# Optimization experiments

Measured on AMD Instinct MI355X. Metric: run time of the kernel, lower is better.

The kernel has to match this reference:

```python
import jax, jax.numpy as jnp
import numpy as np

B, L, H = 2, 4096, 1024
ED, N, R, K = 2048, 16, 64, 4


def setup_inputs() -> dict:
    key = jax.random.key(0)
    ks = jax.random.split(key, 8)
    w = lambda i, shape, s=0.02: jax.random.normal(ks[i], shape, jnp.float32) * s
    # dt bias initialized like Mamba: inv-softplus of dt ~ logU(1e-3, 1e-1)
    dt = jnp.exp(jax.random.uniform(ks[7], (ED,)) * (np.log(0.1) - np.log(0.001)) + np.log(0.001))
    dt = jnp.clip(dt, 1e-4)
    inv_dt = dt + jnp.log(-jnp.expm1(-dt))
    A = jnp.broadcast_to(jnp.arange(1, N + 1, dtype=jnp.float32), (ED, N))
    return dict(
        x=jax.random.normal(ks[0], (B, L, H), jnp.float32),
        in_proj_w=w(1, (2 * ED, H)),
        conv_w=w(2, (ED, K), 0.2),
        conv_b=jnp.zeros((ED,), jnp.float32),
        x_proj_w=w(3, (R + 2 * N, ED)),
        dt_w=w(4, (ED, R), 64 ** -0.5),
        dt_b=inv_dt,
        A_log=jnp.log(A),
        D=jnp.ones((ED,), jnp.float32),
        out_proj_w=w(5, (H, ED)),
    )


def reference(x, in_proj_w, conv_w, conv_b, x_proj_w, dt_w, dt_b, A_log, D, out_proj_w):
    Bq, Lq, Hq = x.shape
    EDq, Kq = conv_w.shape
    Rq = dt_w.shape[1]
    Nq = A_log.shape[1]

    # in_proj -> [B, L, 2*ED]; chunk into hidden_states and gate
    xz = jnp.einsum('blh,eh->ble', x, in_proj_w)
    hs, gate = jnp.split(xz, 2, axis=-1)

    # causal depthwise conv1d along L (padding K-1 on the left), then SiLU
    hs_pad = jnp.pad(hs, ((0, 0), (Kq - 1, 0), (0, 0)))  # [B, L+K-1, ED]
    conv = conv_b
    for k in range(Kq):  # K=4, fixed small loop
        conv = conv + hs_pad[:, k:k + Lq, :] * conv_w[:, k]
    hs = jax.nn.silu(conv)  # [B, L, ED]

    # x_proj -> split into dt (rank R), B (N), C (N)
    ssm = jnp.einsum('ble,pe->blp', hs, x_proj_w)
    dtr, Bm, Cm = jnp.split(ssm, [Rq, Rq + Nq], axis=-1)

    # dt_proj + softplus (delta_softplus=True with delta_bias)
    delta = jax.nn.softplus(jnp.einsum('blr,er->ble', dtr, dt_w) + dt_b)  # [B,L,ED]

    A = -jnp.exp(A_log)  # [ED, N]

    # selective scan: h_t = exp(delta_t*A)*h_{t-1} + delta_t*B_t*u_t ; y_t = <h_t, C_t>
    def step(h, inp):
        d_t, B_t, C_t, u_t = inp  # [B,ED], [B,N], [B,N], [B,ED]
        dA = jnp.exp(d_t[..., None] * A)                      # [B,ED,N]
        h = dA * h + (d_t * u_t)[..., None] * B_t[:, None, :]  # [B,ED,N]
        y = jnp.einsum('ben,bn->be', h, C_t)                   # [B,ED]
        return h, y

    h0 = jnp.zeros((Bq, EDq, Nq), x.dtype)
    xs = (jnp.moveaxis(delta, 1, 0), jnp.moveaxis(Bm, 1, 0),
          jnp.moveaxis(Cm, 1, 0), jnp.moveaxis(hs, 1, 0))
    _, ys = jax.lax.scan(step, h0, xs)  # ys: [L, B, ED]

    y = jnp.moveaxis(ys, 0, 1) + hs * D      # skip term D*u
    y = y * jax.nn.silu(gate)                # gated output
    return jnp.einsum('ble,he->blh', y, out_proj_w)
```

## Files before the change

### kernel.cpp

```cpp
#include <hip/hip_runtime.h>


typedef float f32x4 __attribute__((ext_vector_type(4)));
typedef short short8 __attribute__((ext_vector_type(8)));
typedef unsigned short u16;

#define DEV __device__ __forceinline__

DEV float bf2f(u16 u) {
  union { unsigned int i; float f; } v; v.i = ((unsigned int)u) << 16; return v.f;
}
DEV u16 f2bf(float f) {
  union { float f; unsigned int i; } v; v.f = f;
  return (u16)((v.i + 0x7fffu + ((v.i >> 16) & 1u)) >> 16);
}

DEV void gload_lds16(const void* g, void* l) {
  __builtin_amdgcn_global_load_lds(
      (const __attribute__((address_space(1))) unsigned int*)g,
      (__attribute__((address_space(3))) unsigned int*)l, 16, 0, 0);
}

DEV void mfma_bf16(f32x4& d, short8 a, short8 b) {
  asm("v_mfma_f32_16x16x32_bf16 %0, %1, %2, %0" : "+v"(d) : "v"(a), "v"(b));
}

template <int BM, int BN, int WM, int WN, int BK, int EPI>
__global__ __launch_bounds__(256) void gemm_bt_kernel(
    const u16* __restrict__ A, const u16* __restrict__ Bw,
    int M, int N, int Kd,
    float* __restrict__ o_f32, u16* __restrict__ o_b16a,
    u16* __restrict__ o_b16b, const float* __restrict__ bias,
    float* __restrict__ oB, float* __restrict__ oC)
{
  constexpr int KSN = BK / 32;
  constexpr int CPR = BK / 8;
  constexpr int CPL = (CPR == 8) ? 3 : 2;
  constexpr int MFR = BM / WM / 16;
  constexpr int NFR = BN / WN / 16;
  constexpr int TA = BM * CPR;
  constexpr int TB = BN * CPR;
  __shared__ u16 lds[(BM + BN) * BK];

  const int tid  = threadIdx.x;
  const int wave = tid >> 6;
  const int lane = tid & 63;
  const int row  = lane & 15;
  const int g    = lane >> 4;
  const int key  = (CPR == 8) ? (row & 7) : ((row >> 1) & 3);
  const int rowBase = blockIdx.y * BM;
  const int colBase = blockIdx.x * BN;
  const int WROW = (wave / WN) * (BM / WM);
  const int WCOL = (wave % WN) * (BN / WN);

  f32x4 acc[MFR][NFR];
#pragma unroll
  for (int i = 0; i < MFR; ++i)
#pragma unroll
    for (int j = 0; j < NFR; ++j) acc[i][j] = (f32x4){0.f, 0.f, 0.f, 0.f};

  for (int kk = 0; kk < Kd; kk += BK) {
#pragma unroll
    for (int c0 = 0; c0 < TA; c0 += 256) {
      int ch = c0 + tid;
      if (ch < TA) {
        int r = ch >> CPL;
        int rk = (CPR == 8) ? (r & 7) : ((r >> 1) & 3);
        int gs = (ch & (CPR - 1)) ^ rk;
        gload_lds16(A + (size_t)(rowBase + r) * Kd + kk + gs * 8,
                    (void*)(lds + (c0 + wave * 64) * 8));
      }
    }
#pragma unroll
    for (int c0 = 0; c0 < TB; c0 += 256) {
      int ch = c0 + tid;
      if (ch < TB) {
        int r = ch >> CPL;
        int rk = (CPR == 8) ? (r & 7) : ((r >> 1) & 3);
        int gs = (ch & (CPR - 1)) ^ rk;
        gload_lds16(Bw + (size_t)(colBase + r) * Kd + kk + gs * 8,
                    (void*)(lds + BM * BK + (c0 + wave * 64) * 8));
      }
    }
    __syncthreads();
    short8 af[MFR][KSN], bfr[NFR][KSN];
#pragma unroll
    for (int mi = 0; mi < MFR; ++mi)
#pragma unroll
      for (int ks = 0; ks < KSN; ++ks)
        af[mi][ks] = *(const short8*)(lds + (WROW + mi * 16 + row) * BK +
                                      (((ks * 4 + g) ^ key) * 8));
#pragma unroll
    for (int ni = 0; ni < NFR; ++ni)
#pragma unroll
      for (int ks = 0; ks < KSN; ++ks)
        bfr[ni][ks] = *(const short8*)(lds + BM * BK + (WCOL + ni * 16 + row) * BK +
                                       (((ks * 4 + g) ^ key) * 8));
#pragma unroll
    for (int ks = 0; ks < KSN; ++ks)
#pragma unroll
      for (int mi = 0; mi < MFR; ++mi)
#pragma unroll
        for (int ni = 0; ni < NFR; ++ni)
          mfma_bf16(acc[mi][ni], af[mi][ks], bfr[ni][ks]);
    __syncthreads();
  }

#pragma unroll
  for (int mi = 0; mi < MFR; ++mi) {
#pragma unroll
    for (int ni = 0; ni < NFR; ++ni) {
      const int gcol = colBase + WCOL + ni * 16 + row;
#pragma unroll
      for (int r = 0; r < 4; ++r) {
        const int grow = rowBase + WROW + mi * 16 + g * 4 + r;
        float v = acc[mi][ni][r];
        if constexpr (EPI == 0) {
          o_f32[(size_t)grow * N + gcol] = v;
        } else if constexpr (EPI == 1) {
          if (gcol < 2048) o_b16a[(size_t)grow * 2048 + gcol] = f2bf(v);
          else             o_b16b[(size_t)grow * 2048 + (gcol - 2048)] = f2bf(v);
        } else if constexpr (EPI == 2) {
          if (gcol < 64)      o_b16a[(size_t)grow * 64 + gcol] = f2bf(v);
          else if (gcol < 80) oB[(size_t)grow * 16 + (gcol - 64)] = v;
          else                oC[(size_t)grow * 16 + (gcol - 80)] = v;
        } else {
          float x = v + bias[gcol];
          float sp = (x > 20.f) ? x : __logf(1.f + __expf(x));
          o_b16a[(size_t)grow * N + gcol] = f2bf(sp);
        }
      }
    }
  }
}

DEV void cvt8(const float* in, u16* out, int j) {
  const float4* p = (const float4*)(in + (size_t)j * 8);
  float4 a = p[0], b = p[1];
  float v[8] = {a.x, a.y, a.z, a.w, b.x, b.y, b.z, b.w};
  unsigned o[4];
#pragma unroll
  for (int q = 0; q < 4; ++q)
    o[q] = (unsigned)f2bf(v[2 * q]) | ((unsigned)f2bf(v[2 * q + 1]) << 16);
  *(uint4*)(out + (size_t)j * 8) = make_uint4(o[0], o[1], o[2], o[3]);
}

__global__ __launch_bounds__(256) void cvt_bf16_kernel(
    const float* __restrict__ in, u16* __restrict__ out, int n8)
{
  int i = blockIdx.x * 256 + threadIdx.x;
  if (i >= n8) return;
  cvt8(in, out, i);
}

__global__ __launch_bounds__(256) void cvt4_kernel(
    const float* __restrict__ a0, u16* __restrict__ o0, int n0,
    const float* __restrict__ a1, u16* __restrict__ o1, int n1,
    const float* __restrict__ a2, u16* __restrict__ o2, int n2,
    const float* __restrict__ a3, u16* __restrict__ o3, int n3)
{
  int i = blockIdx.x * 256 + threadIdx.x;
  if (i < n0)                { cvt8(a0, o0, i); return; }
  i -= n0;
  if (i < n1)                { cvt8(a1, o1, i); return; }
  i -= n1;
  if (i < n2)                { cvt8(a2, o2, i); return; }
  i -= n2;
  if (i < n3)                { cvt8(a3, o3, i); }
}

__global__ __launch_bounds__(256) void conv_silu_kernel(
    const u16* __restrict__ hsraw, const float* __restrict__ cw,
    const float* __restrict__ cb, u16* __restrict__ hsb)
{
  int idx = blockIdx.x * 256 + threadIdx.x;
  int e0 = (idx & 255) * 8;
  int t  = (idx >> 8) & 4095;
  int b  = idx >> 20;
  float acc[8];
  float wv[4][8];
#pragma unroll
  for (int j = 0; j < 8; ++j) acc[j] = cb[e0 + j];
#pragma unroll
  for (int k = 0; k < 4; ++k)
#pragma unroll
    for (int j = 0; j < 8; ++j) wv[k][j] = cw[(e0 + j) * 4 + k];
#pragma unroll
  for (int k = 0; k < 4; ++k) {
    int tt = t - 3 + k;
    if (tt < 0) continue;
    uint4 v4 = *(const uint4*)(hsraw + ((size_t)(b * 4096 + tt)) * 2048 + e0);
    unsigned arr[4] = {v4.x, v4.y, v4.z, v4.w};
#pragma unroll
    for (int q = 0; q < 4; ++q) {
      acc[2 * q]     += wv[k][2 * q]     * bf2f((u16)(arr[q] & 0xffffu));
      acc[2 * q + 1] += wv[k][2 * q + 1] * bf2f((u16)(arr[q] >> 16));
    }
  }
  unsigned o[4];
#pragma unroll
  for (int q = 0; q < 4; ++q) {
    float a0 = acc[2 * q], a1 = acc[2 * q + 1];
    a0 = a0 / (1.f + __expf(-a0));
    a1 = a1 / (1.f + __expf(-a1));
    o[q] = (unsigned)f2bf(a0) | ((unsigned)f2bf(a1) << 16);
  }
  *(uint4*)(hsb + ((size_t)(b * 4096 + t)) * 2048 + e0) = make_uint4(o[0], o[1], o[2], o[3]);
}

__global__ __launch_bounds__(256) void scan_phase1(
    const u16* __restrict__ deltab, const u16* __restrict__ hsb,
    const float* __restrict__ Bb, const float* __restrict__ alog,
    float* __restrict__ h_end, float* __restrict__ Ssum)
{
  __shared__ __align__(16) float Bs[64 * 16];
  const int tid = threadIdx.x;
  const int e = blockIdx.x * 256 + tid;
  const int c = blockIdx.y;
  const int b = blockIdx.z;
  const int t0 = c * 64;
  {
    const float* src = Bb + ((size_t)(b * 4096 + t0)) * 16;
#pragma unroll
    for (int k = 0; k < 4; ++k) Bs[tid + k * 256] = src[tid + k * 256];
  }
  float An[16];
  {
    const float4* ap = (const float4*)(alog + e * 16);
#pragma unroll
    for (int q = 0; q < 4; ++q) {
      float4 v = ap[q];
      An[4*q+0] = -__expf(v.x); An[4*q+1] = -__expf(v.y);
      An[4*q+2] = -__expf(v.z); An[4*q+3] = -__expf(v.w);
    }
  }
  __syncthreads();
  float h[16];
#pragma unroll
  for (int n = 0; n < 16; ++n) h[n] = 0.f;
  float sumd = 0.f;
  size_t base = ((size_t)(b * 4096 + t0)) * 2048 + e;
  float dd = bf2f(deltab[base]);
  float uu = bf2f(hsb[base]);
  for (int j = 0; j < 64; ++j) {
    int jn = (j < 63) ? j + 1 : 63;
    float d_nxt = bf2f(deltab[base + (size_t)jn * 2048]);
    float u_nxt = bf2f(hsb[base + (size_t)jn * 2048]);
    const float4* Bv = (const float4*)(Bs + j * 16);
    float4 b0 = Bv[0], b1 = Bv[1], b2 = Bv[2], b3 = Bv[3];
    float Bl[16] = {b0.x,b0.y,b0.z,b0.w, b1.x,b1.y,b1.z,b1.w,
                    b2.x,b2.y,b2.z,b2.w, b3.x,b3.y,b3.z,b3.w};
    sumd += dd;
    float du = dd * uu;
#pragma unroll
    for (int n = 0; n < 16; ++n)
      h[n] = fmaf(__expf(An[n] * dd), h[n], du * Bl[n]);
    dd = d_nxt; uu = u_nxt;
  }
  float* he = h_end + (((size_t)(b * 2048 + e)) * 64 + c) * 16;
#pragma unroll
  for (int q = 0; q < 4; ++q) {
    float4 v = {h[4*q], h[4*q+1], h[4*q+2], h[4*q+3]};
    *(float4*)(he + 4 * q) = v;
  }
  Ssum[((size_t)(b * 2048 + e)) * 64 + c] = sumd;
}

__global__ __launch_bounds__(256) void scan_phase2(
    const float* __restrict__ h_end, const float* __restrict__ Ssum,
    const float* __restrict__ alog, float* __restrict__ h_start)
{
  const int tid = threadIdx.x;
  const int n = tid & 15;
  const int G = blockIdx.x * 16 + (tid >> 4);
  const int e = G & 2047;
  const float An = -__expf(alog[e * 16 + n]);
  size_t hb = (size_t)G * 64 * 16 + n;
  size_t sb = (size_t)G * 64;
  float h = 0.f;
  constexpr int PF = 8;
  float hq[PF], Sq[PF];
#pragma unroll
  for (int j = 0; j < PF; ++j) { hq[j] = h_end[hb + (size_t)j * 16]; Sq[j] = Ssum[sb + j]; }
  for (int c0 = 0; c0 < 64; c0 += PF) {
    float hn[PF], Sn[PF];
#pragma unroll
    for (int j = 0; j < PF; ++j) {
      int cn = c0 + PF + j; cn = (cn < 64) ? cn : 63;
      hn[j] = h_end[hb + (size_t)cn * 16]; Sn[j] = Ssum[sb + cn];
    }
#pragma unroll
    for (int j = 0; j < PF; ++j) {
      h_start[hb + (size_t)(c0 + j) * 16] = h;
      h = fmaf(__expf(An * Sq[j]), h, hq[j]);
    }
#pragma unroll
    for (int j = 0; j < PF; ++j) { hq[j] = hn[j]; Sq[j] = Sn[j]; }
  }
}

__global__ __launch_bounds__(256) void scan_phase3(
    const u16* __restrict__ deltab, const u16* __restrict__ hsb,
    const float* __restrict__ Bb, const float* __restrict__ Cb,
    const float* __restrict__ alog, const float* __restrict__ h_start,
    const float* __restrict__ Dv, u16* __restrict__ gate_y2)
{
  __shared__ __align__(16) float Bs[64 * 16];
  __shared__ __align__(16) float Cs[64 * 16];
  const int tid = threadIdx.x;
  const int e = blockIdx.x * 256 + tid;
  const int c = blockIdx.y;
  const int b = blockIdx.z;
  const int t0 = c * 64;
  {
    const float* srcB = Bb + ((size_t)(b * 4096 + t0)) * 16;
    const float* srcC = Cb + ((size_t)(b * 4096 + t0)) * 16;
#pragma unroll
    for (int k = 0; k < 4; ++k) {
      Bs[tid + k * 256] = srcB[tid + k * 256];
      Cs[tid + k * 256] = srcC[tid + k * 256];
    }
  }
  float An[16];
  {
    const float4* ap = (const float4*)(alog + e * 16);
#pragma unroll
    for (int q = 0; q < 4; ++q) {
      float4 v = ap[q];
      An[4*q+0] = -__expf(v.x); An[4*q+1] = -__expf(v.y);
      An[4*q+2] = -__expf(v.z); An[4*q+3] = -__expf(v.w);
    }
  }
  const float De = Dv[e];
  float h[16];
  {
    const float4* hp = (const float4*)(h_start + (((size_t)(b * 2048 + e)) * 64 + c) * 16);
#pragma unroll
    for (int q = 0; q < 4; ++q) {
      float4 v = hp[q];
      h[4*q+0] = v.x; h[4*q+1] = v.y; h[4*q+2] = v.z; h[4*q+3] = v.w;
    }
  }
  __syncthreads();
  size_t base = ((size_t)(b * 4096 + t0)) * 2048 + e;
  float dd = bf2f(deltab[base]);
  float uu = bf2f(hsb[base]);
  float gg = bf2f(gate_y2[base]);
  for (int j = 0; j < 64; ++j) {
    int jn = (j < 63) ? j + 1 : 63;
    float d_nxt = bf2f(deltab[base + (size_t)jn * 2048]);
    float u_nxt = bf2f(hsb[base + (size_t)jn * 2048]);
    float g_nxt = bf2f(gate_y2[base + (size_t)jn * 2048]);
    const float4* Bv = (const float4*)(Bs + j * 16);
    const float4* Cv = (const float4*)(Cs + j * 16);
    float4 b0 = Bv[0], b1 = Bv[1], b2 = Bv[2], b3 = Bv[3];
    float4 c0v = Cv[0], c1v = Cv[1], c2v = Cv[2], c3v = Cv[3];
    float Bl[16] = {b0.x,b0.y,b0.z,b0.w, b1.x,b1.y,b1.z,b1.w,
                    b2.x,b2.y,b2.z,b2.w, b3.x,b3.y,b3.z,b3.w};
    float Cl[16] = {c0v.x,c0v.y,c0v.z,c0v.w, c1v.x,c1v.y,c1v.z,c1v.w,
                    c2v.x,c2v.y,c2v.z,c2v.w, c3v.x,c3v.y,c3v.z,c3v.w};
    float du = dd * uu;
    float y = 0.f;
#pragma unroll
    for (int n = 0; n < 16; ++n) {
      h[n] = fmaf(__expf(An[n] * dd), h[n], du * Bl[n]);
      y = fmaf(h[n], Cl[n], y);
    }
    float val = (y + uu * De) * (gg / (1.f + __expf(-gg)));
    gate_y2[base + (size_t)j * 2048] = f2bf(val);
    dd = d_nxt; uu = u_nxt; gg = g_nxt;
  }
}

extern "C" void kernel_launch(void* const* d_in, const int* in_sizes, int n_in,
                              void* d_out, int out_size, void* d_ws, size_t ws_size,
                              hipStream_t stream)
{
  const float* x    = (const float*)d_in[0];
  const float* w1   = (const float*)d_in[1];
  const float* cw   = (const float*)d_in[2];
  const float* cb   = (const float*)d_in[3];
  const float* xp   = (const float*)d_in[4];
  const float* dtw  = (const float*)d_in[5];
  const float* dtb  = (const float*)d_in[6];
  const float* alog = (const float*)d_in[7];
  const float* Dp   = (const float*)d_in[8];
  const float* wo   = (const float*)d_in[9];
  float* out = (float*)d_out;
  char* ws = (char*)d_ws;

  const size_t o_xb    = 0;
  const size_t o_wb1   = 16777216;
  const size_t o_xpb   = 25165824;
  const size_t o_dtwb  = 25559040;
  const size_t o_wob   = 25821184;
  const size_t o_hsraw = 30015488;
  const size_t o_gate  = 63569920;
  const size_t o_hsb   = 97124352;
  const size_t o_dtrb  = 130678784;
  const size_t o_Bb    = 131727360;
  const size_t o_Cb    = 132251648;
  const size_t o_delta = 132775936;
  const size_t WS_NEED = o_delta + 67108864 + 262144;
  if (ws_size < WS_NEED) return;

  u16* xb    = (u16*)(ws + o_xb);
  u16* wb1   = (u16*)(ws + o_wb1);
  u16* xpb   = (u16*)(ws + o_xpb);
  u16* dtwb  = (u16*)(ws + o_dtwb);
  u16* wob   = (u16*)(ws + o_wob);
  u16* hsraw = (u16*)(ws + o_hsraw);
  u16* gate  = (u16*)(ws + o_gate);
  u16* hsb   = (u16*)(ws + o_hsb);
  u16* dtrb  = (u16*)(ws + o_dtrb);
  float* Bb    = (float*)(ws + o_Bb);
  float* Cb    = (float*)(ws + o_Cb);
  u16* deltab  = (u16*)(ws + o_delta);
  float* h_end   = (float*)(ws + o_xb);
  float* h_start = (float*)(ws + o_hsraw);
  float* Ssum    = (float*)(ws + o_hsraw + 16777216);

  cvt_bf16_kernel<<<4096, 256, 0, stream>>>(x, xb, 1048576);
  cvt4_kernel<<<3232, 256, 0, stream>>>(
      w1, wb1, 524288, xp, xpb, 24576, dtw, dtwb, 16384, wo, wob, 262144);

  gemm_bt_kernel<128,128,2,2,64,1><<<dim3(32,64), 256, 0, stream>>>(
      xb, wb1, 8192, 4096, 1024, nullptr, hsraw, gate, nullptr, nullptr, nullptr);
  conv_silu_kernel<<<8192, 256, 0, stream>>>(hsraw, cw, cb, hsb);
  gemm_bt_kernel<32,96,2,2,64,2><<<dim3(1,256), 256, 0, stream>>>(
      hsb, xpb, 8192, 96, 2048, nullptr, dtrb, nullptr, nullptr, Bb, Cb);
  gemm_bt_kernel<64,64,2,2,32,3><<<dim3(32,128), 256, 0, stream>>>(
      dtrb, dtwb, 8192, 2048, 64, nullptr, deltab, nullptr, dtb, nullptr, nullptr);

  scan_phase1<<<dim3(8, 64, 2), 256, 0, stream>>>(deltab, hsb, Bb, alog, h_end, Ssum);
  scan_phase2<<<256, 256, 0, stream>>>(h_end, Ssum, alog, h_start);
  scan_phase3<<<dim3(8, 64, 2), 256, 0, stream>>>(
      deltab, hsb, Bb, Cb, alog, h_start, Dp, gate);

  gemm_bt_kernel<128,128,2,2,32,0><<<dim3(8,64), 256, 0, stream>>>(
      gate, wob, 8192, 1024, 2048, out, nullptr, nullptr, nullptr, nullptr, nullptr);
}
```

Baseline: 379.8 us.

## Split-K the x_proj GEMM, merge conversion launches, and enlarge GEMM BK

The narrow x_proj GEMM (N=96, K=2048) previously ran on only 256 blocks. It is now split four ways along K into a partial-sum buffer, and a separate reduction kernel writes dtr (bf16), B and C. The two fp32-to-bf16 conversion kernels are merged into a single launch. BK is raised from 32 to 64 for the dt_proj GEMM (K=64) and for the out_proj GEMM. The split adds an extra kernel launch and a round trip of partial sums through global memory in exchange for more parallelism on the skinny GEMM.

New measurement: 362.0 us. -4.7%, faster.

```diff
diff --git a/kernel.cpp b/kernel.cpp
--- a/kernel.cpp
+++ b/kernel.cpp
@@ -25,13 +25,12 @@
   asm("v_mfma_f32_16x16x32_bf16 %0, %1, %2, %0" : "+v"(d) : "v"(a), "v"(b));
 }
 
-template <int BM, int BN, int WM, int WN, int BK, int EPI>
+template <int BM, int BN, int WM, int WN, int BK, int EPI, int SK = 1>
 __global__ __launch_bounds__(256) void gemm_bt_kernel(
     const u16* __restrict__ A, const u16* __restrict__ Bw,
     int M, int N, int Kd,
     float* __restrict__ o_f32, u16* __restrict__ o_b16a,
-    u16* __restrict__ o_b16b, const float* __restrict__ bias,
-    float* __restrict__ oB, float* __restrict__ oC)
+    u16* __restrict__ o_b16b, const float* __restrict__ bias)
 {
   constexpr int KSN = BK / 32;
   constexpr int CPR = BK / 8;
@@ -49,7 +48,9 @@
   const int g    = lane >> 4;
   const int key  = (CPR == 8) ? (row & 7) : ((row >> 1) & 3);
   const int rowBase = blockIdx.y * BM;
-  const int colBase = blockIdx.x * BN;
+  const int colBase = (SK > 1) ? 0 : blockIdx.x * BN;
+  const int slice = (SK > 1) ? (Kd / SK) : Kd;
+  const int kbeg  = (SK > 1) ? blockIdx.x * slice : 0;
   const int WROW = (wave / WN) * (BM / WM);
   const int WCOL = (wave % WN) * (BN / WN);
 
@@ -59,7 +60,7 @@
 #pragma unroll
     for (int j = 0; j < NFR; ++j) acc[i][j] = (f32x4){0.f, 0.f, 0.f, 0.f};
 
-  for (int kk = 0; kk < Kd; kk += BK) {
+  for (int kk = kbeg; kk < kbeg + slice; kk += BK) {
 #pragma unroll
     for (int c0 = 0; c0 < TA; c0 += 256) {
       int ch = c0 + tid;
@@ -120,18 +121,29 @@
         } else if constexpr (EPI == 1) {
           if (gcol < 2048) o_b16a[(size_t)grow * 2048 + gcol] = f2bf(v);
           else             o_b16b[(size_t)grow * 2048 + (gcol - 2048)] = f2bf(v);
-        } else if constexpr (EPI == 2) {
-          if (gcol < 64)      o_b16a[(size_t)grow * 64 + gcol] = f2bf(v);
-          else if (gcol < 80) oB[(size_t)grow * 16 + (gcol - 64)] = v;
-          else                oC[(size_t)grow * 16 + (gcol - 80)] = v;
-        } else {
+        } else if constexpr (EPI == 3) {
           float x = v + bias[gcol];
           float sp = (x > 20.f) ? x : __logf(1.f + __expf(x));
           o_b16a[(size_t)grow * N + gcol] = f2bf(sp);
+        } else {
+          o_f32[(size_t)blockIdx.x * M * N + (size_t)grow * N + gcol] = v;
         }
       }
     }
   }
+}
+
+__global__ __launch_bounds__(256) void reduce_ssm_kernel(
+    const float* __restrict__ P, u16* __restrict__ dtrb,
+    float* __restrict__ oB, float* __restrict__ oC)
+{
+  const int idx = blockIdx.x * 256 + threadIdx.x;
+  const float s = P[idx] + P[idx + 786432] + P[idx + 2 * 786432] + P[idx + 3 * 786432];
+  const int row = idx / 96;
+  const int col = idx - row * 96;
+  if (col < 64)      dtrb[(size_t)row * 64 + col] = f2bf(s);
+  else if (col < 80) oB[(size_t)row * 16 + (col - 64)] = s;
+  else               oC[(size_t)row * 16 + (col - 80)] = s;
 }
 
 DEV void cvt8(const float* in, u16* out, int j) {
@@ -145,21 +157,16 @@
   *(uint4*)(out + (size_t)j * 8) = make_uint4(o[0], o[1], o[2], o[3]);
 }
 
-__global__ __launch_bounds__(256) void cvt_bf16_kernel(
-    const float* __restrict__ in, u16* __restrict__ out, int n8)
-{
-  int i = blockIdx.x * 256 + threadIdx.x;
-  if (i >= n8) return;
-  cvt8(in, out, i);
-}
-
-__global__ __launch_bounds__(256) void cvt4_kernel(
+__global__ __launch_bounds__(256) void cvt5_kernel(
+    const float* __restrict__ ax, u16* __restrict__ ox, int nx,
     const float* __restrict__ a0, u16* __restrict__ o0, int n0,
     const float* __restrict__ a1, u16* __restrict__ o1, int n1,
     const float* __restrict__ a2, u16* __restrict__ o2, int n2,
     const float* __restrict__ a3, u16* __restrict__ o3, int n3)
 {
   int i = blockIdx.x * 256 + threadIdx.x;
+  if (i < nx)                { cvt8(ax, ox, i); return; }
+  i -= nx;
   if (i < n0)                { cvt8(a0, o0, i); return; }
   i -= n0;
   if (i < n1)                { cvt8(a1, o1, i); return; }
@@ -401,6 +408,7 @@
   const size_t o_Bb    = 131727360;
   const size_t o_Cb    = 132251648;
   const size_t o_delta = 132775936;
+  const size_t o_P     = o_delta + 33554432;
   const size_t WS_NEED = o_delta + 67108864 + 262144;
   if (ws_size < WS_NEED) return;
 
@@ -416,27 +424,29 @@
   float* Bb    = (float*)(ws + o_Bb);
   float* Cb    = (float*)(ws + o_Cb);
   u16* deltab  = (u16*)(ws + o_delta);
+  float* Pbuf  = (float*)(ws + o_P);
   float* h_end   = (float*)(ws + o_xb);
   float* h_start = (float*)(ws + o_hsraw);
   float* Ssum    = (float*)(ws + o_hsraw + 16777216);
 
-  cvt_bf16_kernel<<<4096, 256, 0, stream>>>(x, xb, 1048576);
-  cvt4_kernel<<<3232, 256, 0, stream>>>(
-      w1, wb1, 524288, xp, xpb, 24576, dtw, dtwb, 16384, wo, wob, 262144);
+  cvt5_kernel<<<7328, 256, 0, stream>>>(
+      x, xb, 1048576, w1, wb1, 524288, xp, xpb, 24576,
+      dtw, dtwb, 16384, wo, wob, 262144);
 
   gemm_bt_kernel<128,128,2,2,64,1><<<dim3(32,64), 256, 0, stream>>>(
-      xb, wb1, 8192, 4096, 1024, nullptr, hsraw, gate, nullptr, nullptr, nullptr);
+      xb, wb1, 8192, 4096, 1024, nullptr, hsraw, gate, nullptr);
   conv_silu_kernel<<<8192, 256, 0, stream>>>(hsraw, cw, cb, hsb);
-  gemm_bt_kernel<32,96,2,2,64,2><<<dim3(1,256), 256, 0, stream>>>(
-      hsb, xpb, 8192, 96, 2048, nullptr, dtrb, nullptr, nullptr, Bb, Cb);
-  gemm_bt_kernel<64,64,2,2,32,3><<<dim3(32,128), 256, 0, stream>>>(
-      dtrb, dtwb, 8192, 2048, 64, nullptr, deltab, nullptr, dtb, nullptr, nullptr);
+  gemm_bt_kernel<32,96,2,2,64,4,4><<<dim3(4,256), 256, 0, stream>>>(
+      hsb, xpb, 8192, 96, 2048, Pbuf, nullptr, nullptr, nullptr);
+  reduce_ssm_kernel<<<3072, 256, 0, stream>>>(Pbuf, dtrb, Bb, Cb);
+  gemm_bt_kernel<64,64,2,2,64,3><<<dim3(32,128), 256, 0, stream>>>(
+      dtrb, dtwb, 8192, 2048, 64, nullptr, deltab, nullptr, dtb);
 
   scan_phase1<<<dim3(8, 64, 2), 256, 0, stream>>>(deltab, hsb, Bb, alog, h_end, Ssum);
   scan_phase2<<<256, 256, 0, stream>>>(h_end, Ssum, alog, h_start);
   scan_phase3<<<dim3(8, 64, 2), 256, 0, stream>>>(
       deltab, hsb, Bb, Cb, alog, h_start, Dp, gate);
 
-  gemm_bt_kernel<128,128,2,2,32,0><<<dim3(8,64), 256, 0, stream>>>(
-      gate, wob, 8192, 1024, 2048, out, nullptr, nullptr, nullptr, nullptr, nullptr);
-}
+  gemm_bt_kernel<128,128,2,2,64,0><<<dim3(8,64), 256, 0, stream>>>(
+      gate, wob, 8192, 1024, 2048, out, nullptr, nullptr, nullptr);
+}
```
